# Optimization experiments

Hardware: AMD Instinct MI355X
Metric: run time of the kernel (lower is better)

The kernel has to match this reference:

```python
import jax, jax.numpy as jnp
import numpy as np

N = 100000       # nodes
DEG = 16         # in-degree per node
E = N * DEG      # edges
IN_DIM = 128
H_DIM = 128
NEG_SLOPE = 0.01  # F.leaky_relu default


def setup_inputs() -> dict:
    key = jax.random.key(0)
    ks = jax.random.split(key, 12)
    sc = 0.05
    attr = jax.random.normal(ks[0], (N, IN_DIM), jnp.float32)
    edge_d = jax.random.uniform(ks[1], (E, 1), dtype=jnp.float32)
    edge_src = jax.random.randint(ks[2], (E,), 0, N, dtype=jnp.int32)
    edge_dst = jnp.repeat(jnp.arange(N, dtype=jnp.int32), DEG)  # every node gets DEG msgs
    return {
        "attr": attr,
        "edge_d": edge_d,
        "W_V1": jax.random.normal(ks[3], (1, 1), jnp.float32) * sc,
        "W_W1": jax.random.normal(ks[4], (H_DIM, IN_DIM), jnp.float32) * sc,
        "W_U1": jax.random.normal(ks[5], (H_DIM, IN_DIM), jnp.float32) * sc,
        "W_a1": jax.random.normal(ks[6], (1, 2 * H_DIM + 1), jnp.float32) * sc,
        "W_V2": jax.random.normal(ks[7], (1, 1), jnp.float32) * sc,
        "W_W2": jax.random.normal(ks[8], (H_DIM, H_DIM), jnp.float32) * sc,
        "W_U2": jax.random.normal(ks[9], (H_DIM, H_DIM), jnp.float32) * sc,
        "W_a2": jax.random.normal(ks[10], (1, 2 * H_DIM + 1), jnp.float32) * sc,
        "edge_src": edge_src,
        "edge_dst": edge_dst,
    }


def gat_layer(h, edge_d, edge_src, edge_dst, W_V, W_W, W_U, W_a):
    n = h.shape[0]
    t = edge_d @ W_V.T                      # [E,1] edge feature transform (fcV)
    z = h @ W_W.T                           # [N,H] (fcW)
    z_i = h @ W_U.T                         # [N,H] (fcU)
    Hd = z.shape[1]
    a = W_a[0]                              # [2H+1]
    a_src, a_dst, a_t = a[:Hd], a[Hd:2 * Hd], a[2 * Hd:]
    # attn_fc(concat(z_src, z_dst, t)) decomposed into per-node scores + edge term
    s_src = z @ a_src                       # [N]
    s_dst = z @ a_dst                       # [N]
    e = s_src[edge_src] + s_dst[edge_dst] + (t @ a_t)  # [E]
    e = jax.nn.leaky_relu(e, NEG_SLOPE)
    # per-destination-node softmax over incoming edges (mailbox softmax)
    m = jax.ops.segment_max(e, edge_dst, num_segments=n)
    ex = jnp.exp(e - m[edge_dst])
    denom = jax.ops.segment_sum(ex, edge_dst, num_segments=n)
    alpha = ex / denom[edge_dst]            # [E]
    # weighted neighbor aggregation
    zn = jax.ops.segment_sum(alpha[:, None] * z[edge_src], edge_dst, num_segments=n)
    return jax.nn.relu(z_i + zn)


def reference(attr, edge_d, W_V1, W_W1, W_U1, W_a1, W_V2, W_W2, W_U2, W_a2,
              edge_src, edge_dst):
    h = gat_layer(attr, edge_d, edge_src, edge_dst, W_V1, W_W1, W_U1, W_a1)
    h = gat_layer(h, edge_d, edge_src, edge_dst, W_V2, W_W2, W_U2, W_a2)
    return h
```

## Files before the change

### kernel.cpp

```cpp
#include <hip/hip_runtime.h>

#define N_NODES 100000
#define DEG 16
#define DIM 128
#define NGROUPS 6250
#define GPB 5
#define DBLOCKS (NGROUPS / GPB)

typedef short bf16x8 __attribute__((ext_vector_type(8)));
typedef float f32x4 __attribute__((ext_vector_type(4)));

__device__ __forceinline__ unsigned short f2bf(float f) {
    unsigned int u = __builtin_bit_cast(unsigned int, f);
    u = (u + 0x7fffu + ((u >> 16) & 1u)) >> 16;
    return (unsigned short)u;
}
__device__ __forceinline__ float bf2f(unsigned short h) {
    unsigned int u = ((unsigned int)h) << 16;
    return __builtin_bit_cast(float, u);
}

template <bool F32IN>
__global__ __launch_bounds__(256, 2) void dense_fused(
    const void* __restrict__ hsrc,
    const float* __restrict__ W_W,
    const float* __restrict__ W_U,
    const float* __restrict__ W_a,
    unsigned short* __restrict__ zcat,
    float* __restrict__ s_src0, float* __restrict__ s_src1,
    float* __restrict__ s_dst0, float* __restrict__ s_dst1)
{
    const int wave = threadIdx.x >> 6;
    const int lane = threadIdx.x & 63;
    const int n16 = lane & 15;
    const int quad = lane >> 4;
    const int gbase = blockIdx.x * GPB;

    const float* Wbase = (wave < 2) ? (W_W + (size_t)wave * 64 * DIM)
                                    : (W_U + (size_t)(wave - 2) * 64 * DIM);
    bf16x8 wfrag[4][4];
#pragma unroll
    for (int ct = 0; ct < 4; ct++) {
        const float* wrow = Wbase + (size_t)(ct * 16 + n16) * DIM + quad * 8;
#pragma unroll
        for (int ks = 0; ks < 4; ks++) {
            float4 lo = *(const float4*)(wrow + ks * 32);
            float4 hi = *(const float4*)(wrow + ks * 32 + 4);
            bf16x8 f;
            f[0] = (short)f2bf(lo.x); f[1] = (short)f2bf(lo.y);
            f[2] = (short)f2bf(lo.z); f[3] = (short)f2bf(lo.w);
            f[4] = (short)f2bf(hi.x); f[5] = (short)f2bf(hi.y);
            f[6] = (short)f2bf(hi.z); f[7] = (short)f2bf(hi.w);
            wfrag[ct][ks] = f;
        }
    }

    float4 rf[8];
    bf16x8 rb[2][4];
    bf16x8 hfragA[4], hfragB[4];

    auto issue = [&](int g) {
        int nodebase = (gbase + g) * 16;
        if constexpr (F32IN) {
            const float* hrow = (const float*)hsrc + (size_t)(nodebase + n16) * DIM + quad * 8;
#pragma unroll
            for (int ks = 0; ks < 4; ks++) {
                rf[ks * 2]     = *(const float4*)(hrow + ks * 32);
                rf[ks * 2 + 1] = *(const float4*)(hrow + ks * 32 + 4);
            }
        } else {
            const unsigned short* hrow = (const unsigned short*)hsrc + (size_t)(nodebase + n16) * DIM + quad * 8;
#pragma unroll
            for (int ks = 0; ks < 4; ks++)
                rb[g & 1][ks] = *(const bf16x8*)(hrow + ks * 32);
        }
    };
    auto convert = [&](int g, bf16x8* dst) {
        if constexpr (F32IN) {
#pragma unroll
            for (int ks = 0; ks < 4; ks++) {
                float4 lo = rf[ks * 2], hi = rf[ks * 2 + 1];
                bf16x8 f;
                f[0] = (short)f2bf(lo.x); f[1] = (short)f2bf(lo.y);
                f[2] = (short)f2bf(lo.z); f[3] = (short)f2bf(lo.w);
                f[4] = (short)f2bf(hi.x); f[5] = (short)f2bf(hi.y);
                f[6] = (short)f2bf(hi.z); f[7] = (short)f2bf(hi.w);
                dst[ks] = f;
            }
        } else {
#pragma unroll
            for (int ks = 0; ks < 4; ks++) dst[ks] = rb[g & 1][ks];
        }
    };

    issue(0);
    convert(0, hfragA);

#pragma unroll
    for (int g = 0; g < GPB; g++) {
        const int nodebase = (gbase + g) * 16;
        bf16x8* cur = (g & 1) ? hfragB : hfragA;
        bf16x8* nxt = (g & 1) ? hfragA : hfragB;

        if (g + 1 < GPB) issue(g + 1);

        f32x4 acc[4];
#pragma unroll
        for (int ct = 0; ct < 4; ct++) {
            f32x4 a = {0.f, 0.f, 0.f, 0.f};
#pragma unroll
            for (int ks = 0; ks < 4; ks++)
                a = __builtin_amdgcn_mfma_f32_16x16x32_bf16(wfrag[ct][ks], cur[ks], a, 0, 0, 0);
            acc[ct] = a;
        }

        unsigned short* orow = zcat + (size_t)(nodebase + n16) * 256 + wave * 64 + quad * 4;
#pragma unroll
        for (int ct = 0; ct < 4; ct++) {
            uint2 pk;
            pk.x = (unsigned int)f2bf(acc[ct][0]) | ((unsigned int)f2bf(acc[ct][1]) << 16);
            pk.y = (unsigned int)f2bf(acc[ct][2]) | ((unsigned int)f2bf(acc[ct][3]) << 16);
            *(uint2*)(orow + ct * 16) = pk;
        }

        if (wave < 2) {
            float ps = 0.f, pd = 0.f;
#pragma unroll
            for (int ct = 0; ct < 4; ct++) {
                float4 as = *(const float4*)(W_a + wave * 64 + ct * 16 + quad * 4);
                float4 ad = *(const float4*)(W_a + DIM + wave * 64 + ct * 16 + quad * 4);
                ps += acc[ct][0] * as.x + acc[ct][1] * as.y
                    + acc[ct][2] * as.z + acc[ct][3] * as.w;
                pd += acc[ct][0] * ad.x + acc[ct][1] * ad.y
                    + acc[ct][2] * ad.z + acc[ct][3] * ad.w;
            }
            ps += __shfl_xor(ps, 16); ps += __shfl_xor(ps, 32);
            pd += __shfl_xor(pd, 16); pd += __shfl_xor(pd, 32);
            if (lane < 16) {
                float* sp = wave == 0 ? s_src0 : s_src1;
                float* dp = wave == 0 ? s_dst0 : s_dst1;
                sp[nodebase + lane] = ps;
                dp[nodebase + lane] = pd;
            }
        }

        if (g + 1 < GPB) convert(g + 1, nxt);
    }
}

__global__ __launch_bounds__(256, 3) void aggr_kernel(
    const unsigned short* __restrict__ zcat,
    const float* __restrict__ s_src0, const float* __restrict__ s_src1,
    const float* __restrict__ s_dst0, const float* __restrict__ s_dst1,
    const float* __restrict__ edge_d,
    const int* __restrict__ edge_src,
    const float* __restrict__ W_V,
    const float* __restrict__ W_a,
    unsigned short* __restrict__ out_bf16,
    float* __restrict__ out_f32)
{
    __shared__ float alpha_s[16][DEG];
    __shared__ int   src_s[16][DEG];

    const int t = threadIdx.x;
    const int base = blockIdx.x * 16;

    {
        int nl = t >> 4, j = t & 15;
        int node = base + nl;
        int e = node * DEG + j;
        int s = edge_src[e];
        float coef = W_V[0] * W_a[2 * DIM];
        float x = (s_src0[s] + s_src1[s]) + (s_dst0[node] + s_dst1[node])
                + edge_d[e] * coef;
        x = x > 0.f ? x : 0.01f * x;
        float m = x;
        m = fmaxf(m, __shfl_xor(m, 1));
        m = fmaxf(m, __shfl_xor(m, 2));
        m = fmaxf(m, __shfl_xor(m, 4));
        m = fmaxf(m, __shfl_xor(m, 8));
        float ex = __expf(x - m);
        float d = ex;
        d += __shfl_xor(d, 1); d += __shfl_xor(d, 2);
        d += __shfl_xor(d, 4); d += __shfl_xor(d, 8);
        alpha_s[nl][j] = ex / d;
        src_s[nl][j] = s;
    }
    __syncthreads();

    const int nl = t >> 4;
    const int node = base + nl;
    const int c8 = (t & 15) * 8;

    uint4 raw[DEG];
#pragma unroll
    for (int j = 0; j < DEG; j++)
        raw[j] = *(const uint4*)(zcat + (size_t)src_s[nl][j] * 256 + c8);
    uint4 zr = *(const uint4*)(zcat + (size_t)node * 256 + 128 + c8);

    float acc[8] = {};
#pragma unroll
    for (int j = 0; j < DEG; j++) {
        float a = alpha_s[nl][j];
        acc[0] += a * bf2f((unsigned short)raw[j].x);
        acc[1] += a * bf2f((unsigned short)(raw[j].x >> 16));
        acc[2] += a * bf2f((unsigned short)raw[j].y);
        acc[3] += a * bf2f((unsigned short)(raw[j].y >> 16));
        acc[4] += a * bf2f((unsigned short)raw[j].z);
        acc[5] += a * bf2f((unsigned short)(raw[j].z >> 16));
        acc[6] += a * bf2f((unsigned short)raw[j].w);
        acc[7] += a * bf2f((unsigned short)(raw[j].w >> 16));
    }

    float v[8];
    v[0] = fmaxf(bf2f((unsigned short)zr.x) + acc[0], 0.f);
    v[1] = fmaxf(bf2f((unsigned short)(zr.x >> 16)) + acc[1], 0.f);
    v[2] = fmaxf(bf2f((unsigned short)zr.y) + acc[2], 0.f);
    v[3] = fmaxf(bf2f((unsigned short)(zr.y >> 16)) + acc[3], 0.f);
    v[4] = fmaxf(bf2f((unsigned short)zr.z) + acc[4], 0.f);
    v[5] = fmaxf(bf2f((unsigned short)(zr.z >> 16)) + acc[5], 0.f);
    v[6] = fmaxf(bf2f((unsigned short)zr.w) + acc[6], 0.f);
    v[7] = fmaxf(bf2f((unsigned short)(zr.w >> 16)) + acc[7], 0.f);

    if (out_f32) {
        float* op = out_f32 + (size_t)node * DIM + c8;
        *(float4*)op       = make_float4(v[0], v[1], v[2], v[3]);
        *(float4*)(op + 4) = make_float4(v[4], v[5], v[6], v[7]);
    } else {
        uint4 pk;
        pk.x = (unsigned int)f2bf(v[0]) | ((unsigned int)f2bf(v[1]) << 16);
        pk.y = (unsigned int)f2bf(v[2]) | ((unsigned int)f2bf(v[3]) << 16);
        pk.z = (unsigned int)f2bf(v[4]) | ((unsigned int)f2bf(v[5]) << 16);
        pk.w = (unsigned int)f2bf(v[6]) | ((unsigned int)f2bf(v[7]) << 16);
        *(uint4*)(out_bf16 + (size_t)node * DIM + c8) = pk;
    }
}

extern "C" void kernel_launch(void* const* d_in, const int* in_sizes, int n_in,
                              void* d_out, int out_size, void* d_ws, size_t ws_size,
                              hipStream_t stream) {
    const float* attr     = (const float*)d_in[0];
    const float* edge_d   = (const float*)d_in[1];
    const float* W_V1     = (const float*)d_in[2];
    const float* W_W1     = (const float*)d_in[3];
    const float* W_U1     = (const float*)d_in[4];
    const float* W_a1     = (const float*)d_in[5];
    const float* W_V2     = (const float*)d_in[6];
    const float* W_W2     = (const float*)d_in[7];
    const float* W_U2     = (const float*)d_in[8];
    const float* W_a2     = (const float*)d_in[9];
    const int*   edge_src = (const int*)d_in[10];

    float* out = (float*)d_out;

    char* ws = (char*)d_ws;
    unsigned short* zcat = (unsigned short*)ws;
    unsigned short* h1   = (unsigned short*)(ws + 52u * 1024 * 1024);
    float* s_src0        = (float*)(ws + 78u * 1024 * 1024);
    float* s_src1        = (float*)(ws + 79u * 1024 * 1024);
    float* s_dst0        = (float*)(ws + 80u * 1024 * 1024);
    float* s_dst1        = (float*)(ws + 81u * 1024 * 1024);

    dense_fused<true><<<DBLOCKS, 256, 0, stream>>>(attr, W_W1, W_U1, W_a1, zcat,
                                                   s_src0, s_src1, s_dst0, s_dst1);
    aggr_kernel<<<NGROUPS, 256, 0, stream>>>(zcat, s_src0, s_src1, s_dst0, s_dst1,
                                             edge_d, edge_src, W_V1, W_a1, h1, nullptr);

    dense_fused<false><<<DBLOCKS, 256, 0, stream>>>(h1, W_W2, W_U2, W_a2, zcat,
                                                    s_src0, s_src1, s_dst0, s_dst1);
    aggr_kernel<<<NGROUPS, 256, 0, stream>>>(zcat, s_src0, s_src1, s_dst0, s_dst1,
                                             edge_d, edge_src, W_V2, W_a2, nullptr, out);
}
```

Measured before the change: 342.6 us.

## Prefetch all node groups upfront and shrink groups per block in dense kernel

The dense projection kernel now handles 2 node groups per block instead of 5. It issues every h-row load before loading the weights, replacing the rolling double-buffered issue/convert pipeline. Weight loads are batched two column tiles at a time before conversion to bf16. The aim is more memory-level parallelism and more blocks, at the cost of reloading and converting the weight fragments more often across the grid and holding more registers.

```diff
diff --git a/kernel.cpp b/kernel.cpp
--- a/kernel.cpp
+++ b/kernel.cpp
@@ -4,7 +4,7 @@
 #define DEG 16
 #define DIM 128
 #define NGROUPS 6250
-#define GPB 5
+#define GPB 2
 #define DBLOCKS (NGROUPS / GPB)
 
 typedef short bf16x8 __attribute__((ext_vector_type(8)));
@@ -18,6 +18,14 @@
 __device__ __forceinline__ float bf2f(unsigned short h) {
     unsigned int u = ((unsigned int)h) << 16;
     return __builtin_bit_cast(float, u);
+}
+__device__ __forceinline__ bf16x8 pack_bf16x8(float4 lo, float4 hi) {
+    bf16x8 f;
+    f[0] = (short)f2bf(lo.x); f[1] = (short)f2bf(lo.y);
+    f[2] = (short)f2bf(lo.z); f[3] = (short)f2bf(lo.w);
+    f[4] = (short)f2bf(hi.x); f[5] = (short)f2bf(hi.y);
+    f[6] = (short)f2bf(hi.z); f[7] = (short)f2bf(hi.w);
+    return f;
 }
 
 template <bool F32IN>
@@ -36,73 +44,60 @@
     const int quad = lane >> 4;
     const int gbase = blockIdx.x * GPB;
 
+    float4 hraw[GPB][8];
+    bf16x8 hfrag[GPB][4];
+#pragma unroll
+    for (int g = 0; g < GPB; g++) {
+        int nodebase = (gbase + g) * 16;
+        if constexpr (F32IN) {
+            const float* hrow = (const float*)hsrc + (size_t)(nodebase + n16) * DIM + quad * 8;
+#pragma unroll
+            for (int ks = 0; ks < 4; ks++) {
+                hraw[g][ks * 2]     = *(const float4*)(hrow + ks * 32);
+                hraw[g][ks * 2 + 1] = *(const float4*)(hrow + ks * 32 + 4);
+            }
+        } else {
+            const unsigned short* hrow = (const unsigned short*)hsrc + (size_t)(nodebase + n16) * DIM + quad * 8;
+#pragma unroll
+            for (int ks = 0; ks < 4; ks++)
+                hfrag[g][ks] = *(const bf16x8*)(hrow + ks * 32);
+        }
+    }
+
     const float* Wbase = (wave < 2) ? (W_W + (size_t)wave * 64 * DIM)
                                     : (W_U + (size_t)(wave - 2) * 64 * DIM);
     bf16x8 wfrag[4][4];
 #pragma unroll
-    for (int ct = 0; ct < 4; ct++) {
-        const float* wrow = Wbase + (size_t)(ct * 16 + n16) * DIM + quad * 8;
-#pragma unroll
-        for (int ks = 0; ks < 4; ks++) {
-            float4 lo = *(const float4*)(wrow + ks * 32);
-            float4 hi = *(const float4*)(wrow + ks * 32 + 4);
-            bf16x8 f;
-            f[0] = (short)f2bf(lo.x); f[1] = (short)f2bf(lo.y);
-            f[2] = (short)f2bf(lo.z); f[3] = (short)f2bf(lo.w);
-            f[4] = (short)f2bf(hi.x); f[5] = (short)f2bf(hi.y);
-            f[6] = (short)f2bf(hi.z); f[7] = (short)f2bf(hi.w);
-            wfrag[ct][ks] = f;
-        }
-    }
-
-    float4 rf[8];
-    bf16x8 rb[2][4];
-    bf16x8 hfragA[4], hfragB[4];
-
-    auto issue = [&](int g) {
-        int nodebase = (gbase + g) * 16;
-        if constexpr (F32IN) {
-            const float* hrow = (const float*)hsrc + (size_t)(nodebase + n16) * DIM + quad * 8;
+    for (int half = 0; half < 2; half++) {
+        float4 wraw[2][4][2];
+#pragma unroll
+        for (int c = 0; c < 2; c++) {
+            int ct = half * 2 + c;
+            const float* wrow = Wbase + (size_t)(ct * 16 + n16) * DIM + quad * 8;
 #pragma unroll
             for (int ks = 0; ks < 4; ks++) {
-                rf[ks * 2]     = *(const float4*)(hrow + ks * 32);
-                rf[ks * 2 + 1] = *(const float4*)(hrow + ks * 32 + 4);
-            }
-        } else {
-            const unsigned short* hrow = (const unsigned short*)hsrc + (size_t)(nodebase + n16) * DIM + quad * 8;
-#pragma unroll
-            for (int ks = 0; ks < 4; ks++)
-                rb[g & 1][ks] = *(const bf16x8*)(hrow + ks * 32);
-        }
-    };
-    auto convert = [&](int g, bf16x8* dst) {
-        if constexpr (F32IN) {
-#pragma unroll
-            for (int ks = 0; ks < 4; ks++) {
-                float4 lo = rf[ks * 2], hi = rf[ks * 2 + 1];
-                bf16x8 f;
-                f[0] = (short)f2bf(lo.x); f[1] = (short)f2bf(lo.y);
-                f[2] = (short)f2bf(lo.z); f[3] = (short)f2bf(lo.w);
-                f[4] = (short)f2bf(hi.x); f[5] = (short)f2bf(hi.y);
-                f[6] = (short)f2bf(hi.z); f[7] = (short)f2bf(hi.w);
-                dst[ks] = f;
-            }
-        } else {
-#pragma unroll
-            for (int ks = 0; ks < 4; ks++) dst[ks] = rb[g & 1][ks];
-        }
-    };
-
-    issue(0);
-    convert(0, hfragA);
+                wraw[c][ks][0] = *(const float4*)(wrow + ks * 32);
+                wraw[c][ks][1] = *(const float4*)(wrow + ks * 32 + 4);
+            }
+        }
+#pragma unroll
+        for (int c = 0; c < 2; c++)
+#pragma unroll
+            for (int ks = 0; ks < 4; ks++)
+                wfrag[half * 2 + c][ks] = pack_bf16x8(wraw[c][ks][0], wraw[c][ks][1]);
+    }
+
+    if constexpr (F32IN) {
+#pragma unroll
+        for (int g = 0; g < GPB; g++)
+#pragma unroll
+            for (int ks = 0; ks < 4; ks++)
+                hfrag[g][ks] = pack_bf16x8(hraw[g][ks * 2], hraw[g][ks * 2 + 1]);
+    }
 
 #pragma unroll
     for (int g = 0; g < GPB; g++) {
         const int nodebase = (gbase + g) * 16;
-        bf16x8* cur = (g & 1) ? hfragB : hfragA;
-        bf16x8* nxt = (g & 1) ? hfragA : hfragB;
-
-        if (g + 1 < GPB) issue(g + 1);
 
         f32x4 acc[4];
 #pragma unroll
@@ -110,7 +105,7 @@
             f32x4 a = {0.f, 0.f, 0.f, 0.f};
 #pragma unroll
             for (int ks = 0; ks < 4; ks++)
-                a = __builtin_amdgcn_mfma_f32_16x16x32_bf16(wfrag[ct][ks], cur[ks], a, 0, 0, 0);
+                a = __builtin_amdgcn_mfma_f32_16x16x32_bf16(wfrag[ct][ks], hfrag[g][ks], a, 0, 0, 0);
             acc[ct] = a;
         }
 
@@ -143,8 +138,6 @@
                 dp[nodebase + lane] = pd;
             }
         }
-
-        if (g + 1 < GPB) convert(g + 1, nxt);
     }
 }
 
```

Result: slower. 387.6 us (+13.1%).
